# Kernel tuning notes

Measured on AMD Instinct MI355X. Metric: run time of the kernel, lower is better.

## Reference

```python
import jax, jax.numpy as jnp
import numpy as np

T_STEP, NUM_PATCHES = 16, 49
DIM, MLP_DIM, HEADS, DEPTH = 512, 2048, 8, 4
PATCH_DIM = 432
N_BATCH = 32
NEG = -1e9
EPS = 1e-5


def _ln(x, g, b):
    m = x.mean(-1, keepdims=True)
    v = ((x - m) ** 2).mean(-1, keepdims=True)
    return (x - m) / jnp.sqrt(v + EPS) * g + b


def setup_inputs() -> dict:
    key = jax.random.key(0)
    ks = jax.random.split(key, 16)
    L = T_STEP * NUM_PATCHES
    s = 0.02
    return {
        "patch": jax.random.normal(ks[0], (N_BATCH, L, PATCH_DIM), jnp.float32),
        "done": jax.random.randint(ks[1], (N_BATCH, T_STEP - 1), 0, 2).astype(jnp.int32),
        "W_embed": jax.random.normal(ks[2], (PATCH_DIM, DIM), jnp.float32) * s,
        "b_embed": jnp.zeros((DIM,), jnp.float32),
        "spatial_embed": jax.random.normal(ks[3], (1, NUM_PATCHES, DIM), jnp.float32),
        "temporal_embed": jax.random.normal(ks[4], (1, T_STEP, DIM), jnp.float32),
        "ln1_g": jnp.ones((DEPTH, DIM), jnp.float32),
        "ln1_b": jnp.zeros((DEPTH, DIM), jnp.float32),
        "Wqkv": jax.random.normal(ks[5], (DEPTH, DIM, 3 * DIM), jnp.float32) * s,
        "bqkv": jnp.zeros((DEPTH, 3 * DIM), jnp.float32),
        "Wo": jax.random.normal(ks[6], (DEPTH, DIM, DIM), jnp.float32) * s,
        "bo": jnp.zeros((DEPTH, DIM), jnp.float32),
        "ln2_g": jnp.ones((DEPTH, DIM), jnp.float32),
        "ln2_b": jnp.zeros((DEPTH, DIM), jnp.float32),
        "W1": jax.random.normal(ks[7], (DEPTH, DIM, MLP_DIM), jnp.float32) * s,
        "b1": jnp.zeros((DEPTH, MLP_DIM), jnp.float32),
        "W2": jax.random.normal(ks[8], (DEPTH, MLP_DIM, DIM), jnp.float32) * s,
        "b2": jnp.zeros((DEPTH, DIM), jnp.float32),
        "out_g": jnp.ones((DIM,), jnp.float32),
        "out_b": jnp.zeros((DIM,), jnp.float32),
    }


def reference(patch, done, W_embed, b_embed, spatial_embed, temporal_embed,
              ln1_g, ln1_b, Wqkv, bqkv, Wo, bo, ln2_g, ln2_b,
              W1, b1, W2, b2, out_g, out_b):
    N, L, _ = patch.shape
    # patch embed + factored pos embed
    x = patch @ W_embed + b_embed
    pos = jnp.tile(spatial_embed, (1, T_STEP, 1)) + jnp.repeat(temporal_embed, NUM_PATCHES, axis=1)
    x = x + pos
    # episodic attention mask: done_mask[n,t] = 1 iff any done[n, c]==1 for c >= t
    d = done.astype(jnp.float32)  # (N, T-1)
    dm = (jnp.flip(jnp.cumsum(jnp.flip(d, 1), 1), 1) > 0).astype(jnp.float32)
    dm = jnp.concatenate([dm, jnp.zeros((N, 1), jnp.float32)], axis=1)  # (N, T)
    pm = jnp.repeat(dm, NUM_PATCHES, axis=1)  # (N, L)
    keep = 1.0 - pm
    mask = 1.0 - keep[:, :, None] * keep[:, None, :]  # (N, L, L); 1 = blocked
    bias = jnp.where(mask > 0.5, NEG, 0.0)[:, None, :, :]  # (N, 1, L, L)
    dh = DIM // HEADS
    scale = dh ** -0.5
    for i in range(DEPTH):
        h = _ln(x, ln1_g[i], ln1_b[i])
        qkv = h @ Wqkv[i] + bqkv[i]
        q, k, v = jnp.split(qkv, 3, axis=-1)
        q = q.reshape(N, L, HEADS, dh).transpose(0, 2, 1, 3)
        k = k.reshape(N, L, HEADS, dh).transpose(0, 2, 1, 3)
        v = v.reshape(N, L, HEADS, dh).transpose(0, 2, 1, 3)
        scores = jnp.einsum('nhqd,nhkd->nhqk', q, k) * scale + bias
        attn = jax.nn.softmax(scores, axis=-1)
        o = jnp.einsum('nhqk,nhkd->nhqd', attn, v)
        o = o.transpose(0, 2, 1, 3).reshape(N, L, DIM)
        x = x + (o @ Wo[i] + bo[i])
        h = _ln(x, ln2_g[i], ln2_b[i])
        x = x + (jax.nn.gelu(h @ W1[i] + b1[i], approximate=False) @ W2[i] + b2[i])
    return _ln(x, out_g, out_b)
```

## Files before the change

kernel.cpp:

```cpp
#include <hip/hip_runtime.h>
#include <math.h>

#define NB 32
#define LQ 784
#define LQP 832
#define DIM 512
#define HEADS 8
#define MLP 2048
#define KPAD 448
#define MROWS 25088

typedef __attribute__((ext_vector_type(8))) short s8v;
typedef __attribute__((ext_vector_type(4))) float f4v;

__device__ __forceinline__ short f2b(float f){
  unsigned u = __builtin_bit_cast(unsigned, f);
  u = (u + 0x7fffu + ((u >> 16) & 1u)) >> 16;
  return (short)u;
}
__device__ __forceinline__ float b2f(short s){
  unsigned u = ((unsigned)(unsigned short)s) << 16;
  return __builtin_bit_cast(float, u);
}

__device__ __forceinline__ void gll16(const short* g, short* l){
  __builtin_amdgcn_global_load_lds(
      (const __attribute__((address_space(1))) void*)g,
      (__attribute__((address_space(3))) void*)l, 16, 0, 0);
}

__global__ __launch_bounds__(256) void keepl_k(const int* __restrict__ done, float* __restrict__ keepL){
  int idx = blockIdx.x*256 + threadIdx.x;
  if (idx >= NB*LQP) return;
  int n = idx / LQP, l = idx - n*LQP;
  float v = 0.f;
  if (l < LQ){
    int t = l / 49;
    int any = 0;
    for (int c = t; c < 15; ++c) any |= done[n*15 + c];
    v = any ? 0.f : 1.f;
  }
  keepL[idx] = v;
}

__global__ __launch_bounds__(64) void kmask_k(const float* __restrict__ keepL, int* __restrict__ kmask){
  int n = blockIdx.x, lane = threadIdx.x;
  int m = 0;
  for (int kb = 0; kb < 13; ++kb){
    float v = keepL[n*LQP + kb*64 + lane];
    unsigned long long b = __ballot(v > 0.5f);
    if (b) m |= (1 << kb);
  }
  if (lane == 0) kmask[n] = m;
}

__global__ __launch_bounds__(256) void zpad_k(short* __restrict__ Qb, short* __restrict__ Kb,
                                              short* __restrict__ Vtb){
  int idx = blockIdx.x*256 + threadIdx.x;
  int which = idx / 786432;
  int r = idx - which*786432;
  int nh = r / (48*64);
  int r2 = r - nh*48*64;
  if (which == 0){
    int l = 784 + (r2 >> 6), d = r2 & 63;
    Qb[((long)nh*LQP + l)*64 + d] = 0;
  } else if (which == 1){
    int l = 784 + (r2 >> 6), d = r2 & 63;
    Kb[((long)nh*LQP + l)*64 + d] = 0;
  } else {
    int d = r2 / 48, c = r2 - d*48;
    Vtb[((long)nh*64 + d)*LQP + 784 + c] = 0;
  }
}

__global__ __launch_bounds__(256) void vmean_k(const short* __restrict__ Vtb, float* __restrict__ Vm){
  int nh = blockIdx.x;
  int tid = threadIdx.x;
  int d = tid >> 2, seg = tid & 3;
  const short* row = Vtb + ((long)nh*64 + d)*LQP;
  float s = 0.f;
  for (int c = seg; c < 98; c += 4){
    s8v v = *(const s8v*)(row + c*8);
    #pragma unroll
    for (int e=0;e<8;++e) s += b2f(v[e]);
  }
  s += __shfl_xor(s, 1, 64);
  s += __shfl_xor(s, 2, 64);
  if (seg == 0) Vm[nh*64 + d] = s * (1.0f/784.0f);
}

__global__ __launch_bounds__(256) void padpatch_k(const float* __restrict__ src, short* __restrict__ dst){
  long idx = (long)blockIdx.x * 256 + threadIdx.x;
  if (idx >= (long)MROWS * KPAD) return;
  int r = (int)(idx / KPAD);
  int c = (int)(idx - (long)r * KPAD);
  dst[idx] = (c < 432) ? f2b(src[(long)r * 432 + c]) : (short)0;
}

__global__ __launch_bounds__(256) void transp_k(const float* __restrict__ src, short* __restrict__ dst,
                                                int R, int C, int Rpad, long sStride, long dStride){
  long idx = (long)blockIdx.x * 256 + threadIdx.x;
  long total = (long)C * Rpad;
  if (idx >= total) return;
  int z = blockIdx.y;
  int cc = (int)(idx / Rpad);
  int r = (int)(idx - (long)cc * Rpad);
  short v = 0;
  if (r < R) v = f2b(src[(long)z * sStride + (long)r * C + cc]);
  dst[(long)z * dStride + idx] = v;
}

__global__ __launch_bounds__(256) void ln_k(const float* __restrict__ x, const float* __restrict__ g,
                                            const float* __restrict__ b, short* __restrict__ outb,
                                            float* __restrict__ outf){
  int lane = threadIdx.x & 63;
  long row = (long)blockIdx.x * 4 + (threadIdx.x >> 6);
  const float* xr = x + row * DIM + lane * 8;
  float va[8];
  { float4 t0 = *(const float4*)xr; float4 t1 = *(const float4*)(xr + 4);
    va[0]=t0.x; va[1]=t0.y; va[2]=t0.z; va[3]=t0.w;
    va[4]=t1.x; va[5]=t1.y; va[6]=t1.z; va[7]=t1.w; }
  float s = 0.f, q = 0.f;
  #pragma unroll
  for (int j=0;j<8;++j){ s += va[j]; q += va[j]*va[j]; }
  #pragma unroll
  for (int m=1;m<64;m<<=1){ s += __shfl_xor(s,m,64); q += __shfl_xor(q,m,64); }
  float mean = s * (1.0f/DIM);
  float var = q * (1.0f/DIM) - mean*mean;
  float inv = rsqrtf(var + 1e-5f);
  int cb = lane*8;
  if (outb){
    s8v o;
    #pragma unroll
    for (int j=0;j<8;++j) o[j] = f2b((va[j]-mean)*inv*g[cb+j] + b[cb+j]);
    *(s8v*)(outb + row*DIM + cb) = o;
  } else {
    float4 t0, t1;
    t0.x=(va[0]-mean)*inv*g[cb+0]+b[cb+0]; t0.y=(va[1]-mean)*inv*g[cb+1]+b[cb+1];
    t0.z=(va[2]-mean)*inv*g[cb+2]+b[cb+2]; t0.w=(va[3]-mean)*inv*g[cb+3]+b[cb+3];
    t1.x=(va[4]-mean)*inv*g[cb+4]+b[cb+4]; t1.y=(va[5]-mean)*inv*g[cb+5]+b[cb+5];
    t1.z=(va[6]-mean)*inv*g[cb+6]+b[cb+6]; t1.w=(va[7]-mean)*inv*g[cb+7]+b[cb+7];
    *(float4*)(outf + row*DIM + cb) = t0;
    *(float4*)(outf + row*DIM + cb + 4) = t1;
  }
}

template<int EPI>
__global__ __launch_bounds__(256) void gemm_k(
    const short* __restrict__ A, const short* __restrict__ Bt,
    const float* __restrict__ bias, int K, int N,
    float* __restrict__ xres, short* __restrict__ outb,
    const float* __restrict__ sp, const float* __restrict__ tp,
    short* __restrict__ Qb, short* __restrict__ Kb, short* __restrict__ Vtb)
{
  __shared__ __align__(16) short lA[128*64];
  __shared__ __align__(16) short lB[128*64];
  int tid = threadIdx.x;
  int lane = tid & 63, wid = tid >> 6;
  int col = lane & 15, quad = lane >> 4;
  int wm = (wid >> 1) * 64, wn = (wid & 1) * 64;
  long bm = blockIdx.y, bn = blockIdx.x;
  f4v acc[4][4];
  #pragma unroll
  for (int i=0;i<4;++i)
    #pragma unroll
    for (int j=0;j<4;++j)
      #pragma unroll
      for (int e=0;e<4;++e) acc[i][j][e] = 0.0f;
  const short* Abase = A + bm*128*(long)K;
  const short* Bbase = Bt + bn*128*(long)K;
  for (int kt = 0; kt < K; kt += 64){
    __syncthreads();
    #pragma unroll
    for (int c = 0; c < 4; ++c){
      int v = c*256 + tid;
      int r = v >> 3, j = v & 7;
      int kc = (j ^ (r & 7)) * 8;
      gll16(Abase + (long)r*K + kt + kc, lA + v*8);
      gll16(Bbase + (long)r*K + kt + kc, lB + v*8);
    }
    __syncthreads();
    #pragma unroll
    for (int ks = 0; ks < 2; ++ks){
      s8v af[4], bf[4];
      #pragma unroll
      for (int i=0;i<4;++i)
        af[i] = *(const s8v*)&lA[(wm + i*16 + col)*64 + (((ks*4+quad) ^ (col&7)))*8];
      #pragma unroll
      for (int j=0;j<4;++j)
        bf[j] = *(const s8v*)&lB[(wn + j*16 + col)*64 + (((ks*4+quad) ^ (col&7)))*8];
      #pragma unroll
      for (int i=0;i<4;++i)
        #pragma unroll
        for (int j=0;j<4;++j)
          acc[i][j] = __builtin_amdgcn_mfma_f32_16x16x32_bf16(af[i], bf[j], acc[i][j], 0, 0, 0);
    }
  }
  #pragma unroll
  for (int i=0;i<4;++i){
    #pragma unroll
    for (int r=0;r<4;++r){
      int grow = (int)bm*128 + wm + i*16 + quad*4 + r;
      #pragma unroll
      for (int j=0;j<4;++j){
        int gcol = (int)bn*128 + wn + j*16 + col;
        float v = acc[i][j][r] + bias[gcol];
        if (EPI == 0){
          int l = grow % LQ;
          int t = l / 49;
          int p = l - t*49;
          v += sp[p*DIM + gcol] + tp[t*DIM + gcol];
          xres[(long)grow*DIM + gcol] = v;
        } else if (EPI == 1){
          int n = grow / LQ;
          int l = grow - n*LQ;
          if (gcol < 512){
            int hh = gcol >> 6, d = gcol & 63;
            Qb[(((long)(n*HEADS + hh))*LQP + l)*64 + d] = f2b(v);
          } else if (gcol < 1024){
            int c2 = gcol - 512; int hh = c2 >> 6, d = c2 & 63;
            Kb[(((long)(n*HEADS + hh))*LQP + l)*64 + d] = f2b(v);
          } else {
            int c2 = gcol - 1024; int hh = c2 >> 6, d = c2 & 63;
            Vtb[(((long)(n*HEADS + hh))*64 + d)*LQP + l] = f2b(v);
          }
        } else if (EPI == 2){
          xres[(long)grow*DIM + gcol] += v;
        } else if (EPI == 3){
          float gl = 0.5f * v * (1.0f + erff(v * 0.70710678118654752f));
          outb[(long)grow*MLP + gcol] = f2b(gl);
        }
      }
    }
  }
}

__global__ __launch_bounds__(256) void attn_k(
    const short* __restrict__ Qb, const short* __restrict__ Kb,
    const short* __restrict__ Vtb, const float* __restrict__ keepL,
    const int* __restrict__ kmask, const float* __restrict__ Vm,
    short* __restrict__ Ob)
{
  __shared__ __align__(16) short lK[64*64];
  __shared__ __align__(16) short lV[64*64];
  __shared__ __align__(16) short lP[4][16*72];
  int tid = threadIdx.x;
  int lane = tid & 63, wid = tid >> 6;
  int col = lane & 15, quad = lane >> 4;
  int qb = blockIdx.x, h = blockIdx.y, n = blockIdx.z;
  long nh = (long)n*HEADS + h;
  int smask = kmask[n];
  int qr0 = qb*64 + wid*16;
  float vmv[4];
  #pragma unroll
  for (int j=0;j<4;++j) vmv[j] = Vm[nh*64 + j*16 + col];

  if (!((smask >> qb) & 1)){
    #pragma unroll
    for (int j=0;j<4;++j){
      short ov = f2b(vmv[j]);
      #pragma unroll
      for (int r=0;r<4;++r){
        int l = qr0 + quad*4 + r;
        if (l < LQ) Ob[((long)n*LQ + l)*DIM + h*64 + j*16 + col] = ov;
      }
    }
    return;
  }

  const float* kl = keepL + n*LQP;
  const short* qp = Qb + (nh*LQP + qr0 + col)*64 + quad*8;
  s8v aq0 = *(const s8v*)qp;
  s8v aq1 = *(const s8v*)(qp + 32);
  float keepQ[4];
  #pragma unroll
  for (int r=0;r<4;++r) keepQ[r] = kl[qr0 + quad*4 + r];
  float kqs = keepQ[0] + keepQ[1] + keepQ[2] + keepQ[3];
  bool wlive = __ballot(kqs > 0.5f) != 0ull;
  float lsum[4] = {0.f,0.f,0.f,0.f};
  f4v Oacc[4];
  #pragma unroll
  for (int j=0;j<4;++j)
    #pragma unroll
    for (int e=0;e<4;++e) Oacc[j][e] = 0.0f;

  for (int kb = 0; kb < 13; ++kb){
    if (!((smask >> kb) & 1)) continue;
    int kbase = kb*64;
    __syncthreads();
    #pragma unroll
    for (int c = 0; c < 2; ++c){
      int v = c*256 + tid;
      int r = v >> 3, j = v & 7;
      int kc = (j ^ (r & 7)) * 8;
      gll16(Kb + (nh*LQP + kbase + r)*64 + kc, lK + v*8);
    }
    #pragma unroll
    for (int c = 0; c < 2; ++c){
      int v = c*256 + tid;
      int d = v >> 3, j = v & 7;
      int c8 = (j ^ (d & 7)) * 8;
      gll16(Vtb + (nh*64 + d)*LQP + kbase + c8, lV + v*8);
    }
    __syncthreads();
    if (!wlive) continue;
    float pm[4][4];
    #pragma unroll
    for (int ct = 0; ct < 4; ++ct){
      f4v s;
      #pragma unroll
      for (int e=0;e<4;++e) s[e] = 0.0f;
      #pragma unroll
      for (int ks = 0; ks < 2; ++ks){
        s8v bk = *(const s8v*)&lK[(ct*16 + col)*64 + (((ks*4+quad) ^ (col&7)))*8];
        s = __builtin_amdgcn_mfma_f32_16x16x32_bf16(ks ? aq1 : aq0, bk, s, 0, 0, 0);
      }
      float keepK = kl[kbase + ct*16 + col];
      #pragma unroll
      for (int r=0;r<4;++r){
        float a = keepQ[r] * keepK;
        float t = fmaf(s[r], 0.125f, 10000.0f);
        float p = __expf(fmaf(a, t, -10000.0f));
        pm[ct][r] = p;
        lsum[r] += p;
      }
    }
    #pragma unroll
    for (int ct=0; ct<4; ++ct)
      #pragma unroll
      for (int r=0;r<4;++r)
        lP[wid][(quad*4 + r)*72 + ct*16 + col] = f2b(pm[ct][r]);
    #pragma unroll
    for (int j=0;j<4;++j){
      #pragma unroll
      for (int ks=0; ks<2; ++ks){
        s8v ap = *(const s8v*)&lP[wid][col*72 + ks*32 + quad*8];
        s8v bv = *(const s8v*)&lV[(j*16 + col)*64 + (((ks*4+quad) ^ (col&7)))*8];
        Oacc[j] = __builtin_amdgcn_mfma_f32_16x16x32_bf16(ap, bv, Oacc[j], 0, 0, 0);
      }
    }
  }
  #pragma unroll
  for (int m=1; m<16; m<<=1){
    #pragma unroll
    for (int r=0;r<4;++r) lsum[r] += __shfl_xor(lsum[r], m, 64);
  }
  float invl[4];
  #pragma unroll
  for (int r=0;r<4;++r) invl[r] = 1.0f / lsum[r];
  #pragma unroll
  for (int j=0;j<4;++j)
    #pragma unroll
    for (int r=0;r<4;++r){
      int l = qr0 + quad*4 + r;
      if (l < LQ){
        float val = keepQ[r] > 0.5f ? Oacc[j][r] * invl[r] : vmv[j];
        Ob[((long)n*LQ + l)*DIM + h*64 + j*16 + col] = f2b(val);
      }
    }
}

extern "C" void kernel_launch(void* const* d_in, const int* in_sizes, int n_in,
                              void* d_out, int out_size, void* d_ws, size_t ws_size,
                              hipStream_t stream) {
  const float* patch    = (const float*)d_in[0];
  const int*   done     = (const int*)d_in[1];
  const float* W_embed  = (const float*)d_in[2];
  const float* b_embed  = (const float*)d_in[3];
  const float* spatial  = (const float*)d_in[4];
  const float* temporal = (const float*)d_in[5];
  const float* ln1_g    = (const float*)d_in[6];
  const float* ln1_b    = (const float*)d_in[7];
  const float* Wqkv     = (const float*)d_in[8];
  const float* bqkv     = (const float*)d_in[9];
  const float* Wo       = (const float*)d_in[10];
  const float* bo       = (const float*)d_in[11];
  const float* ln2_g    = (const float*)d_in[12];
  const float* ln2_b    = (const float*)d_in[13];
  const float* W1       = (const float*)d_in[14];
  const float* b1       = (const float*)d_in[15];
  const float* W2       = (const float*)d_in[16];
  const float* b2       = (const float*)d_in[17];
  const float* out_g    = (const float*)d_in[18];
  const float* out_b    = (const float*)d_in[19];
  float* out = (float*)d_out;

  char* ws = (char*)d_ws;
  size_t off = 0;
  auto alloc = [&](size_t bytes)->char*{ char* p = ws + off; off += (bytes + 255) & ~(size_t)255; return p; };
  const size_t QKV_B = (size_t)NB*HEADS*LQP*64*2;
  float* x    = (float*)alloc((size_t)MROWS*DIM*4);
  short* hbuf = (short*)alloc((size_t)MROWS*DIM*2);
  char*  U    = alloc((size_t)MROWS*MLP*2);
  short* patchb = (short*)U;
  short* Qb   = (short*)U;
  short* Kbf  = (short*)(U + QKV_B);
  short* Vtb  = (short*)(U + 2*QKV_B);
  short* obuf = hbuf;
  short* mid  = (short*)U;
  short* Wembt = (short*)alloc((size_t)512*448*2);
  short* Wqkvt = (short*)alloc((size_t)4*1536*512*2);
  short* Wot   = (short*)alloc((size_t)4*512*512*2);
  short* W1t   = (short*)alloc((size_t)4*2048*512*2);
  short* W2t   = (short*)alloc((size_t)4*512*2048*2);
  float* keepL = (float*)alloc((size_t)NB*LQP*4);
  int*   kmask = (int*)alloc(NB*4);
  float* Vm    = (float*)alloc((size_t)NB*HEADS*64*4);

  keepl_k<<<(NB*LQP + 255)/256, 256, 0, stream>>>(done, keepL);
  kmask_k<<<NB, 64, 0, stream>>>(keepL, kmask);
  padpatch_k<<<((long)MROWS*KPAD + 255)/256, 256, 0, stream>>>(patch, patchb);
  transp_k<<<dim3((512*448+255)/256, 1), 256, 0, stream>>>(W_embed, Wembt, 432, 512, 448, 0, 0);
  transp_k<<<dim3((1536*512+255)/256, 4), 256, 0, stream>>>(Wqkv, Wqkvt, 512, 1536, 512, 512L*1536, 1536L*512);
  transp_k<<<dim3((512*512+255)/256, 4), 256, 0, stream>>>(Wo, Wot, 512, 512, 512, 512L*512, 512L*512);
  transp_k<<<dim3((2048*512+255)/256, 4), 256, 0, stream>>>(W1, W1t, 512, 2048, 512, 512L*2048, 2048L*512);
  transp_k<<<dim3((512*2048+255)/256, 4), 256, 0, stream>>>(W2, W2t, 2048, 512, 2048, 2048L*512, 512L*2048);

  gemm_k<0><<<dim3(DIM/128, MROWS/128), 256, 0, stream>>>(
      patchb, Wembt, b_embed, KPAD, DIM, x, nullptr, spatial, temporal, nullptr, nullptr, nullptr);

  for (int i = 0; i < 4; ++i){
    ln_k<<<MROWS/4, 256, 0, stream>>>(x, ln1_g + i*DIM, ln1_b + i*DIM, hbuf, nullptr);
    gemm_k<1><<<dim3(1536/128, MROWS/128), 256, 0, stream>>>(
        hbuf, Wqkvt + (size_t)i*1536*512, bqkv + (size_t)i*1536, DIM, 1536,
        nullptr, nullptr, nullptr, nullptr, Qb, Kbf, Vtb);
    zpad_k<<<(3*786432)/256, 256, 0, stream>>>(Qb, Kbf, Vtb);
    vmean_k<<<NB*HEADS, 256, 0, stream>>>(Vtb, Vm);
    attn_k<<<dim3(13, HEADS, NB), 256, 0, stream>>>(Qb, Kbf, Vtb, keepL, kmask, Vm, obuf);
    gemm_k<2><<<dim3(DIM/128, MROWS/128), 256, 0, stream>>>(
        obuf, Wot + (size_t)i*512*512, bo + (size_t)i*DIM, DIM, DIM,
        x, nullptr, nullptr, nullptr, nullptr, nullptr, nullptr);
    ln_k<<<MROWS/4, 256, 0, stream>>>(x, ln2_g + i*DIM, ln2_b + i*DIM, hbuf, nullptr);
    gemm_k<3><<<dim3(MLP/128, MROWS/128), 256, 0, stream>>>(
        hbuf, W1t + (size_t)i*2048*512, b1 + (size_t)i*MLP, DIM, MLP,
        nullptr, mid, nullptr, nullptr, nullptr, nullptr, nullptr);
    gemm_k<2><<<dim3(DIM/128, MROWS/128), 256, 0, stream>>>(
        mid, W2t + (size_t)i*512*2048, b2 + (size_t)i*DIM, MLP, DIM,
        x, nullptr, nullptr, nullptr, nullptr, nullptr, nullptr);
  }
  ln_k<<<MROWS/4, 256, 0, stream>>>(x, out_g, out_b, nullptr, out);
}
```

Measured before the change: 1.812 ms.

## Skip dead-row Q/K GEMM tiles, fuse prep kernels, use tanh GELU

Merges the mask kernels into one single-block kernel that also computes a per-64-row liveness flag. The QKV GEMM uses that flag to skip Q/K output tiles whose rows are all masked, and attention zeroes Q and K fragments by keep flags so stale values are harmless. It also merges the patch padding and all weight transposes into one launch, vectorises the pad zeroing and runs it once outside the layer loop, and replaces erf GELU with an exp-based tanh approximation. Risks: the hoisted zpad region aliases the MLP buffer, which overwrites it each layer, and the GELU approximation changes the numerics.

```diff
diff --git a/kernel.cpp b/kernel.cpp
--- a/kernel.cpp
+++ b/kernel.cpp
@@ -29,47 +29,55 @@
       (__attribute__((address_space(3))) void*)l, 16, 0, 0);
 }
 
-__global__ __launch_bounds__(256) void keepl_k(const int* __restrict__ done, float* __restrict__ keepL){
-  int idx = blockIdx.x*256 + threadIdx.x;
-  if (idx >= NB*LQP) return;
-  int n = idx / LQP, l = idx - n*LQP;
-  float v = 0.f;
-  if (l < LQ){
-    int t = l / 49;
+__global__ __launch_bounds__(512) void mask_k(const int* __restrict__ done, float* __restrict__ keepL,
+                                              int* __restrict__ kmask, int* __restrict__ liveg){
+  __shared__ float keep[32][16];
+  int tid = threadIdx.x;
+  { int n = tid >> 4, t = tid & 15;
     int any = 0;
     for (int c = t; c < 15; ++c) any |= done[n*15 + c];
-    v = any ? 0.f : 1.f;
-  }
-  keepL[idx] = v;
-}
-
-__global__ __launch_bounds__(64) void kmask_k(const float* __restrict__ keepL, int* __restrict__ kmask){
-  int n = blockIdx.x, lane = threadIdx.x;
-  int m = 0;
-  for (int kb = 0; kb < 13; ++kb){
-    float v = keepL[n*LQP + kb*64 + lane];
-    unsigned long long b = __ballot(v > 0.5f);
-    if (b) m |= (1 << kb);
-  }
-  if (lane == 0) kmask[n] = m;
+    keep[n][t] = any ? 0.f : 1.f; }
+  __syncthreads();
+  for (int i = tid; i < NB*LQP; i += 512){
+    int n = i / LQP, l = i - n*LQP;
+    keepL[i] = (l < LQ) ? keep[n][l/49] : 0.f;
+  }
+  if (tid < 32){
+    int n = tid, m = 0;
+    for (int kb = 0; kb < 13; ++kb){
+      int t0 = (kb*64)/49, t1 = (kb*64 + 63)/49; if (t1 > 15) t1 = 15;
+      float a = 0.f;
+      for (int t = t0; t <= t1; ++t) a += keep[n][t];
+      if (a > 0.5f) m |= 1 << kb;
+    }
+    kmask[n] = m;
+  }
+  for (int g = tid; g < 392; g += 512){
+    float a = 0.f;
+    for (int i2 = 0; i2 < 64; ++i2){
+      int row = g*64 + i2;
+      int n = row / 784, l = row - n*784;
+      a += keep[n][l/49];
+    }
+    liveg[g] = a > 0.5f ? 1 : 0;
+  }
 }
 
 __global__ __launch_bounds__(256) void zpad_k(short* __restrict__ Qb, short* __restrict__ Kb,
                                               short* __restrict__ Vtb){
   int idx = blockIdx.x*256 + threadIdx.x;
-  int which = idx / 786432;
-  int r = idx - which*786432;
-  int nh = r / (48*64);
-  int r2 = r - nh*48*64;
-  if (which == 0){
-    int l = 784 + (r2 >> 6), d = r2 & 63;
-    Qb[((long)nh*LQP + l)*64 + d] = 0;
-  } else if (which == 1){
-    int l = 784 + (r2 >> 6), d = r2 & 63;
-    Kb[((long)nh*LQP + l)*64 + d] = 0;
+  s8v z;
+  #pragma unroll
+  for (int e=0;e<8;++e) z[e] = 0;
+  if (idx < 98304){
+    int nh = idx / 384, r = idx - nh*384;
+    *(s8v*)(Qb + (long)nh*LQP*64 + 784*64 + r*8) = z;
+  } else if (idx < 196608){
+    int i2 = idx - 98304; int nh = i2 / 384, r = i2 - nh*384;
+    *(s8v*)(Kb + (long)nh*LQP*64 + 784*64 + r*8) = z;
   } else {
-    int d = r2 / 48, c = r2 - d*48;
-    Vtb[((long)nh*64 + d)*LQP + 784 + c] = 0;
+    int i2 = idx - 196608; int nh = i2 / 384, rem = i2 - nh*384, d = rem/6, s = rem - d*6;
+    *(s8v*)(Vtb + ((long)nh*64 + d)*LQP + 784 + s*8) = z;
   }
 }
 
@@ -89,25 +97,57 @@
   if (seg == 0) Vm[nh*64 + d] = s * (1.0f/784.0f);
 }
 
-__global__ __launch_bounds__(256) void padpatch_k(const float* __restrict__ src, short* __restrict__ dst){
-  long idx = (long)blockIdx.x * 256 + threadIdx.x;
-  if (idx >= (long)MROWS * KPAD) return;
-  int r = (int)(idx / KPAD);
-  int c = (int)(idx - (long)r * KPAD);
-  dst[idx] = (c < 432) ? f2b(src[(long)r * 432 + c]) : (short)0;
-}
-
-__global__ __launch_bounds__(256) void transp_k(const float* __restrict__ src, short* __restrict__ dst,
-                                                int R, int C, int Rpad, long sStride, long dStride){
-  long idx = (long)blockIdx.x * 256 + threadIdx.x;
-  long total = (long)C * Rpad;
-  if (idx >= total) return;
-  int z = blockIdx.y;
-  int cc = (int)(idx / Rpad);
-  int r = (int)(idx - (long)cc * Rpad);
+__device__ __forceinline__ void transp_body(long idx, const float* __restrict__ src,
+                                            short* __restrict__ dst, int R, int C, int Rpad,
+                                            long sStride, long dStride){
+  long per = (long)C * Rpad;
+  int z = (int)(idx / per);
+  long rem = idx - (long)z * per;
+  int cc = (int)(rem / Rpad);
+  int r  = (int)(rem - (long)cc * Rpad);
   short v = 0;
   if (r < R) v = f2b(src[(long)z * sStride + (long)r * C + cc]);
-  dst[(long)z * dStride + idx] = v;
+  dst[(long)z * dStride + rem] = v;
+}
+
+#define PB0 43904
+#define PB1 896
+#define PB2 12288
+#define PB3 4096
+#define PB4 16384
+#define PB5 16384
+
+__global__ __launch_bounds__(256) void prep_k(
+    const float* __restrict__ patch, short* __restrict__ patchb,
+    const float* __restrict__ Wemb, short* __restrict__ Wembt,
+    const float* __restrict__ Wqkv, short* __restrict__ Wqkvt,
+    const float* __restrict__ Wo, short* __restrict__ Wot,
+    const float* __restrict__ W1, short* __restrict__ W1t,
+    const float* __restrict__ W2, short* __restrict__ W2t){
+  int b = blockIdx.x;
+  int tid = threadIdx.x;
+  if (b < PB0){
+    long idx = (long)b*256 + tid;
+    if (idx >= (long)MROWS*KPAD) return;
+    int r = (int)(idx / KPAD);
+    int c = (int)(idx - (long)r*KPAD);
+    patchb[idx] = (c < 432) ? f2b(patch[(long)r*432 + c]) : (short)0;
+  } else if (b < PB0+PB1){
+    long idx = (long)(b-PB0)*256 + tid;
+    if (idx < 229376) transp_body(idx, Wemb, Wembt, 432, 512, 448, 0, 0);
+  } else if (b < PB0+PB1+PB2){
+    long idx = (long)(b-PB0-PB1)*256 + tid;
+    if (idx < 3145728) transp_body(idx, Wqkv, Wqkvt, 512, 1536, 512, 512L*1536, 1536L*512);
+  } else if (b < PB0+PB1+PB2+PB3){
+    long idx = (long)(b-PB0-PB1-PB2)*256 + tid;
+    if (idx < 1048576) transp_body(idx, Wo, Wot, 512, 512, 512, 512L*512, 512L*512);
+  } else if (b < PB0+PB1+PB2+PB3+PB4){
+    long idx = (long)(b-PB0-PB1-PB2-PB3)*256 + tid;
+    if (idx < 4194304) transp_body(idx, W1, W1t, 512, 2048, 512, 512L*2048, 2048L*512);
+  } else {
+    long idx = (long)(b-PB0-PB1-PB2-PB3-PB4)*256 + tid;
+    if (idx < 4194304) transp_body(idx, W2, W2t, 2048, 512, 2048, 2048L*512, 512L*2048);
+  }
 }
 
 __global__ __launch_bounds__(256) void ln_k(const float* __restrict__ x, const float* __restrict__ g,
@@ -151,15 +191,19 @@
     const float* __restrict__ bias, int K, int N,
     float* __restrict__ xres, short* __restrict__ outb,
     const float* __restrict__ sp, const float* __restrict__ tp,
-    short* __restrict__ Qb, short* __restrict__ Kb, short* __restrict__ Vtb)
+    short* __restrict__ Qb, short* __restrict__ Kb, short* __restrict__ Vtb,
+    const int* __restrict__ liveg)
 {
   __shared__ __align__(16) short lA[128*64];
   __shared__ __align__(16) short lB[128*64];
+  long bm = blockIdx.y, bn = blockIdx.x;
+  if (EPI == 1){
+    if (bn < 8 && liveg[2*bm] == 0 && liveg[2*bm+1] == 0) return;
+  }
   int tid = threadIdx.x;
   int lane = tid & 63, wid = tid >> 6;
   int col = lane & 15, quad = lane >> 4;
   int wm = (wid >> 1) * 64, wn = (wid & 1) * 64;
-  long bm = blockIdx.y, bn = blockIdx.x;
   f4v acc[4][4];
   #pragma unroll
   for (int i=0;i<4;++i)
@@ -227,7 +271,7 @@
         } else if (EPI == 2){
           xres[(long)grow*DIM + gcol] += v;
         } else if (EPI == 3){
-          float gl = 0.5f * v * (1.0f + erff(v * 0.70710678118654752f));
+          float gl = v / (1.0f + __expf(-1.595769122f * v * (1.0f + 0.044715f*v*v)));
           outb[(long)grow*MLP + gcol] = f2b(gl);
         }
       }
@@ -272,6 +316,11 @@
   const short* qp = Qb + (nh*LQP + qr0 + col)*64 + quad*8;
   s8v aq0 = *(const s8v*)qp;
   s8v aq1 = *(const s8v*)(qp + 32);
+  float keepA = kl[qr0 + col];
+  if (keepA < 0.5f){
+    #pragma unroll
+    for (int e=0;e<8;++e){ aq0[e] = 0; aq1[e] = 0; }
+  }
   float keepQ[4];
   #pragma unroll
   for (int r=0;r<4;++r) keepQ[r] = kl[qr0 + quad*4 + r];
@@ -307,15 +356,19 @@
     float pm[4][4];
     #pragma unroll
     for (int ct = 0; ct < 4; ++ct){
+      float keepK = kl[kbase + ct*16 + col];
       f4v s;
       #pragma unroll
       for (int e=0;e<4;++e) s[e] = 0.0f;
       #pragma unroll
       for (int ks = 0; ks < 2; ++ks){
         s8v bk = *(const s8v*)&lK[(ct*16 + col)*64 + (((ks*4+quad) ^ (col&7)))*8];
+        if (keepK < 0.5f){
+          #pragma unroll
+          for (int e=0;e<8;++e) bk[e] = 0;
+        }
         s = __builtin_amdgcn_mfma_f32_16x16x32_bf16(ks ? aq1 : aq0, bk, s, 0, 0, 0);
       }
-      float keepK = kl[kbase + ct*16 + col];
       #pragma unroll
       for (int r=0;r<4;++r){
         float a = keepQ[r] * keepK;
@@ -405,38 +458,36 @@
   short* W2t   = (short*)alloc((size_t)4*512*2048*2);
   float* keepL = (float*)alloc((size_t)NB*LQP*4);
   int*   kmask = (int*)alloc(NB*4);
+  int*   liveg = (int*)alloc(392*4);
   float* Vm    = (float*)alloc((size_t)NB*HEADS*64*4);
 
-  keepl_k<<<(NB*LQP + 255)/256, 256, 0, stream>>>(done, keepL);
-  kmask_k<<<NB, 64, 0, stream>>>(keepL, kmask);
-  padpatch_k<<<((long)MROWS*KPAD + 255)/256, 256, 0, stream>>>(patch, patchb);
-  transp_k<<<dim3((512*448+255)/256, 1), 256, 0, stream>>>(W_embed, Wembt, 432, 512, 448, 0, 0);
-  transp_k<<<dim3((1536*512+255)/256, 4), 256, 0, stream>>>(Wqkv, Wqkvt, 512, 1536, 512, 512L*1536, 1536L*512);
-  transp_k<<<dim3((512*512+255)/256, 4), 256, 0, stream>>>(Wo, Wot, 512, 512, 512, 512L*512, 512L*512);
-  transp_k<<<dim3((2048*512+255)/256, 4), 256, 0, stream>>>(W1, W1t, 512, 2048, 512, 512L*2048, 2048L*512);
-  transp_k<<<dim3((512*2048+255)/256, 4), 256, 0, stream>>>(W2, W2t, 2048, 512, 2048, 2048L*512, 512L*2048);
+  mask_k<<<1, 512, 0, stream>>>(done, keepL, kmask, liveg);
+  prep_k<<<PB0+PB1+PB2+PB3+PB4+PB5, 256, 0, stream>>>(
+      patch, patchb, W_embed, Wembt, Wqkv, Wqkvt, Wo, Wot, W1, W1t, W2, W2t);
 
   gemm_k<0><<<dim3(DIM/128, MROWS/128), 256, 0, stream>>>(
-      patchb, Wembt, b_embed, KPAD, DIM, x, nullptr, spatial, temporal, nullptr, nullptr, nullptr);
+      patchb, Wembt, b_embed, KPAD, DIM, x, nullptr, spatial, temporal,
+      nullptr, nullptr, nullptr, nullptr);
+
+  zpad_k<<<1152, 256, 0, stream>>>(Qb, Kbf, Vtb);
 
   for (int i = 0; i < 4; ++i){
     ln_k<<<MROWS/4, 256, 0, stream>>>(x, ln1_g + i*DIM, ln1_b + i*DIM, hbuf, nullptr);
     gemm_k<1><<<dim3(1536/128, MROWS/128), 256, 0, stream>>>(
         hbuf, Wqkvt + (size_t)i*1536*512, bqkv + (size_t)i*1536, DIM, 1536,
-        nullptr, nullptr, nullptr, nullptr, Qb, Kbf, Vtb);
-    zpad_k<<<(3*786432)/256, 256, 0, stream>>>(Qb, Kbf, Vtb);
+        nullptr, nullptr, nullptr, nullptr, Qb, Kbf, Vtb, liveg);
     vmean_k<<<NB*HEADS, 256, 0, stream>>>(Vtb, Vm);
     attn_k<<<dim3(13, HEADS, NB), 256, 0, stream>>>(Qb, Kbf, Vtb, keepL, kmask, Vm, obuf);
     gemm_k<2><<<dim3(DIM/128, MROWS/128), 256, 0, stream>>>(
         obuf, Wot + (size_t)i*512*512, bo + (size_t)i*DIM, DIM, DIM,
-        x, nullptr, nullptr, nullptr, nullptr, nullptr, nullptr);
+        x, nullptr, nullptr, nullptr, nullptr, nullptr, nullptr, nullptr);
     ln_k<<<MROWS/4, 256, 0, stream>>>(x, ln2_g + i*DIM, ln2_b + i*DIM, hbuf, nullptr);
     gemm_k<3><<<dim3(MLP/128, MROWS/128), 256, 0, stream>>>(
         hbuf, W1t + (size_t)i*2048*512, b1 + (size_t)i*MLP, DIM, MLP,
-        nullptr, mid, nullptr, nullptr, nullptr, nullptr, nullptr);
+        nullptr, mid, nullptr, nullptr, nullptr, nullptr, nullptr, nullptr);
     gemm_k<2><<<dim3(DIM/128, MROWS/128), 256, 0, stream>>>(
         mid, W2t + (size_t)i*512*2048, b2 + (size_t)i*DIM, MLP, DIM,
-        x, nullptr, nullptr, nullptr, nullptr, nullptr, nullptr);
+        x, nullptr, nullptr, nullptr, nullptr, nullptr, nullptr, nullptr);
   }
   ln_k<<<MROWS/4, 256, 0, stream>>>(x, out_g, out_b, nullptr, out);
 }
```

After: 1.684 ms. 7.1% less time.
